# Kernel optimization log

Hardware: AMD Instinct MI355X
Metric: run time of the kernel (lower is better)

Reference implementation:

```python
import jax, jax.numpy as jnp
import numpy as np

VOCAB = 1_000_000      # max_vocabulary_size_per_gpu (use_hashtable=False -> direct index)
EMB = 64               # embedding_vec_size
BATCH = 4096
SLOTS = 26             # slot_num
MAX_NNZ = 10           # max_nnz per slot
COMBINER = "mean"     # 'mean' or 'sum'


def setup_inputs() -> dict:
    key = jax.random.key(0)
    k1, k2, k3 = jax.random.split(key, 3)
    keys = jax.random.randint(k1, (BATCH, SLOTS, MAX_NNZ), 0, VOCAB, dtype=jnp.int32)
    # validity mask: models SparseTensor ragged structure (padded to max_nnz)
    mask = jax.random.uniform(k2, (BATCH, SLOTS, MAX_NNZ)) < 0.6
    # default initializer: random_uniform(-0.05, 0.05)
    table = jax.random.uniform(k3, (VOCAB, EMB), minval=-0.05, maxval=0.05, dtype=jnp.float32)
    return {"keys": keys, "mask": mask, "table": table}


def reference(keys, mask, table):
    # gather: [B, S, N, E]; zero out padded slots
    gathered = table[keys] * mask[..., None].astype(table.dtype)
    summed = jnp.sum(gathered, axis=2)  # [B, S, E]
    if COMBINER == "mean":
        counts = jnp.maximum(jnp.sum(mask, axis=2), 1).astype(table.dtype)  # [B, S]
        return summed / counts[..., None]
    return summed
```

## Files before the change

kernel.cpp:

```cpp
#include <hip/hip_runtime.h>

#define BATCH   4096
#define SLOTS   26
#define MAX_NNZ 10
#define EMB     64
#define ROWS    (BATCH * SLOTS)

typedef float floatx2 __attribute__((ext_vector_type(2)));

__global__ __launch_bounds__(256, 8) void emb_fwd_kernel(
    const int*   __restrict__ keys,
    const int*   __restrict__ mask,
    const float* __restrict__ table,
    float*       __restrict__ out)
{
    int tid = blockIdx.x * blockDim.x + threadIdx.x;
    int row = tid >> 5;
    int e2  = tid & 31;
    if (row >= ROWS) return;

    const int* kp = keys + row * MAX_NNZ;
    const int* mp = mask + row * MAX_NNZ;

    unsigned off[MAX_NNZ];
    int cnt = 0;
#pragma unroll
    for (int j = 0; j < MAX_NNZ; ++j) {
        int k = kp[j];
        int m = mp[j];
        cnt += (m != 0);
        off[j] = ((unsigned)(m ? k : 0)) << 8;
    }

    const char* tb = (const char*)table;
    unsigned e8 = (unsigned)e2 * 8u;

    floatx2 r0 = *(const floatx2*)(tb + e8);
    floatx2 v[MAX_NNZ];
#pragma unroll
    for (int j = 0; j < MAX_NNZ; ++j) {
        v[j] = *(const floatx2*)(tb + (off[j] + e8));
    }

    floatx2 s01 = v[0] + v[1];
    floatx2 s23 = v[2] + v[3];
    floatx2 s45 = v[4] + v[5];
    floatx2 s67 = v[6] + v[7];
    floatx2 s89 = v[8] + v[9];
    floatx2 acc = ((s01 + s23) + (s45 + s67)) + s89;

    float miss = (float)(MAX_NNZ - cnt);
    float inv  = 1.0f / (float)(cnt > 0 ? cnt : 1);
    acc = (acc - miss * r0) * inv;

    floatx2* op = (floatx2*)(out + (size_t)row * EMB) + e2;
    __builtin_nontemporal_store(acc, op);
}

extern "C" void kernel_launch(void* const* d_in, const int* in_sizes, int n_in,
                              void* d_out, int out_size, void* d_ws, size_t ws_size,
                              hipStream_t stream) {
    const int*   keys  = (const int*)d_in[0];
    const int*   mask  = (const int*)d_in[1];
    const float* table = (const float*)d_in[2];
    float*       out   = (float*)d_out;

    const int threads_per_row = 32;
    const int block = 256;
    const long long total_threads = (long long)ROWS * threads_per_row;
    const int grid = (int)((total_threads + block - 1) / block);

    emb_fwd_kernel<<<grid, block, 0, stream>>>(keys, mask, table, out);
}
```

Baseline: 338.1 us.

## Persistent waves with software-pipelined key prefetch and double-buffered gathers

Replaces the one-row-per-32-threads launch with a fixed grid of 2048 persistent waves, each handling two rows per step over 26 steps. Keys and masks are loaded two steps ahead as int2 vectors, and table gathers for the next row pair are issued before the current pair is reduced and stored. The aim is to hide gather and key-load latency through explicit overlap within each wave instead of relying on massive occupancy. The cost is higher register pressure, fewer resident waves, and a fixed grid size tied to the problem shape.

```diff
diff --git a/kernel.cpp b/kernel.cpp
--- a/kernel.cpp
+++ b/kernel.cpp
@@ -5,56 +5,93 @@
 #define MAX_NNZ 10
 #define EMB     64
 #define ROWS    (BATCH * SLOTS)
+#define RPW     2
+#define NSLOTB  (ROWS / RPW)
+#define NBLK    512
+#define WPB     4
+#define NWAVE   (NBLK * WPB)
+#define NS      (NSLOTB / NWAVE)
+#define PAIRS   (NS / 2)
 
 typedef float floatx2 __attribute__((ext_vector_type(2)));
+typedef int   intx2   __attribute__((ext_vector_type(2)));
 
-__global__ __launch_bounds__(256, 8) void emb_fwd_kernel(
+__global__ __launch_bounds__(256) void emb_fwd_kernel(
     const int*   __restrict__ keys,
     const int*   __restrict__ mask,
     const float* __restrict__ table,
     float*       __restrict__ out)
 {
-    int tid = blockIdx.x * blockDim.x + threadIdx.x;
-    int row = tid >> 5;
-    int e2  = tid & 31;
-    if (row >= ROWS) return;
-
-    const int* kp = keys + row * MAX_NNZ;
-    const int* mp = mask + row * MAX_NNZ;
-
-    unsigned off[MAX_NNZ];
-    int cnt = 0;
-#pragma unroll
-    for (int j = 0; j < MAX_NNZ; ++j) {
-        int k = kp[j];
-        int m = mp[j];
-        cnt += (m != 0);
-        off[j] = ((unsigned)(m ? k : 0)) << 8;
-    }
+    const int lane = threadIdx.x & 63;
+    const int gw   = (blockIdx.x * blockDim.x + threadIdx.x) >> 6;
+    const int half = lane >> 5;
+    const int e2   = lane & 31;
 
     const char* tb = (const char*)table;
-    unsigned e8 = (unsigned)e2 * 8u;
+    const floatx2 r0 = *(const floatx2*)(tb + e2 * 8);
 
-    floatx2 r0 = *(const floatx2*)(tb + e8);
-    floatx2 v[MAX_NNZ];
+    intx2 krA[5], mrA[5], krB[5], mrB[5];
+    unsigned off[MAX_NNZ];
+    floatx2  vA[MAX_NNZ], vB[MAX_NNZ];
+    float cntA, cntB;
+
+    auto kload = [&](intx2* kr, intx2* mr, int s) {
+        const size_t r = (size_t)(gw + s * NWAVE) * RPW + half;
+        const intx2* kp = (const intx2*)(keys + r * MAX_NNZ);
+        const intx2* mp = (const intx2*)(mask + r * MAX_NNZ);
 #pragma unroll
-    for (int j = 0; j < MAX_NNZ; ++j) {
-        v[j] = *(const floatx2*)(tb + (off[j] + e8));
+        for (int t = 0; t < 5; ++t) { kr[t] = kp[t]; mr[t] = mp[t]; }
+    };
+
+    auto conv = [&](const intx2* kr, const intx2* mr, float& cnt) {
+        int c = 0;
+#pragma unroll
+        for (int j = 0; j < MAX_NNZ; ++j) {
+            int k = kr[j >> 1][j & 1];
+            int m = mr[j >> 1][j & 1];
+            c += (m != 0);
+            off[j] = ((unsigned)(m != 0 ? k : 0)) << 8;
+        }
+        cnt = (float)c;
+    };
+
+    auto gissue = [&](floatx2* v) {
+#pragma unroll
+        for (int j = 0; j < MAX_NNZ; ++j)
+            v[j] = *(const floatx2*)(tb + (off[j] + (unsigned)(e2 * 8)));
+    };
+
+    auto finish = [&](const floatx2* v, float cnt, int s) {
+        floatx2 acc = (floatx2){0.f, 0.f};
+#pragma unroll
+        for (int j = 0; j < MAX_NNZ; ++j) acc += v[j];
+        float c = cnt > 0.f ? cnt : 1.f;
+        floatx2 res = (acc - (10.f - cnt) * r0) * (1.0f / c);
+        const size_t r = (size_t)(gw + s * NWAVE) * RPW + half;
+        __builtin_nontemporal_store(res, (floatx2*)(out + r * EMB + e2 * 2));
+    };
+
+    kload(krA, mrA, 0);
+    conv(krA, mrA, cntA);
+    kload(krB, mrB, 1);
+    gissue(vA);
+    conv(krB, mrB, cntB);
+    kload(krA, mrA, 2);
+    gissue(vB);
+    kload(krB, mrB, 3);
+
+#pragma unroll 1
+    for (int t = 0; t < PAIRS; ++t) {
+        const int a = 2 * t, b = 2 * t + 1;
+
+        finish(vA, cntA, a);
+        if (a + 2 < NS) { conv(krA, mrA, cntA); gissue(vA); }
+        if (a + 4 < NS) kload(krA, mrA, a + 4);
+
+        finish(vB, cntB, b);
+        if (b + 2 < NS) { conv(krB, mrB, cntB); gissue(vB); }
+        if (b + 4 < NS) kload(krB, mrB, b + 4);
     }
-
-    floatx2 s01 = v[0] + v[1];
-    floatx2 s23 = v[2] + v[3];
-    floatx2 s45 = v[4] + v[5];
-    floatx2 s67 = v[6] + v[7];
-    floatx2 s89 = v[8] + v[9];
-    floatx2 acc = ((s01 + s23) + (s45 + s67)) + s89;
-
-    float miss = (float)(MAX_NNZ - cnt);
-    float inv  = 1.0f / (float)(cnt > 0 ? cnt : 1);
-    acc = (acc - miss * r0) * inv;
-
-    floatx2* op = (floatx2*)(out + (size_t)row * EMB) + e2;
-    __builtin_nontemporal_store(acc, op);
 }
 
 extern "C" void kernel_launch(void* const* d_in, const int* in_sizes, int n_in,
@@ -65,10 +102,5 @@
     const float* table = (const float*)d_in[2];
     float*       out   = (float*)d_out;
 
-    const int threads_per_row = 32;
-    const int block = 256;
-    const long long total_threads = (long long)ROWS * threads_per_row;
-    const int grid = (int)((total_threads + block - 1) / block);
-
-    emb_fwd_kernel<<<grid, block, 0, stream>>>(keys, mask, table, out);
+    emb_fwd_kernel<<<NBLK, 256, 0, stream>>>(keys, mask, table, out);
 }
```

After: 338.5 us. No clear change (+0.1%).
